# Performance work log

Hardware: AMD Instinct MI355X
Metric: run time of the kernel (lower is better)

Reference implementation:

```python
import jax, jax.numpy as jnp
import numpy as np


def setup_inputs() -> dict:
    key = jax.random.key(0)
    x = jax.random.uniform(key, (8, 3, 224, 224), dtype=jnp.float32)
    return {"x": x, "T": 100}


def reference(x, T):
    # normalize to [0, 1] using global min/max (as in the torch module)
    xn = (x - x.min()) / (x.max() - x.min() + 1e-8)
    # time-to-first-spike index per element, truncated like .long()
    spike_times = jnp.clip(((1.0 - xn) * (T - 1)).astype(jnp.int32), 0, T - 1)  # [B,C,H,W]
    # one-hot along the new time axis: spikes[b, t, ...] = 1 where t == spike_time
    t_axis = jnp.arange(T, dtype=jnp.int32)  # [T]
    spikes = (spike_times[:, None] == t_axis[None, :, None, None, None]).astype(jnp.float32)
    return spikes  # [B, T, C, H, W]
```

## Files before the change

kernel.cpp:

```cpp
#include <hip/hip_runtime.h>
#include <cfloat>

#define BLK 256
#define RED_BLOCKS 256
#define SPLIT 21

typedef float floatx4 __attribute__((ext_vector_type(4)));

__global__ void k_minmax_partial(const float* __restrict__ x, int n4,
                                 float* __restrict__ partial) {
    const float4* __restrict__ x4 = (const float4*)x;
    float mn = FLT_MAX, mx = -FLT_MAX;
    for (int i = blockIdx.x * blockDim.x + threadIdx.x; i < n4;
         i += gridDim.x * blockDim.x) {
        float4 v = x4[i];
        mn = fminf(mn, fminf(fminf(v.x, v.y), fminf(v.z, v.w)));
        mx = fmaxf(mx, fmaxf(fmaxf(v.x, v.y), fmaxf(v.z, v.w)));
    }
    for (int off = 32; off > 0; off >>= 1) {
        mn = fminf(mn, __shfl_down(mn, off, 64));
        mx = fmaxf(mx, __shfl_down(mx, off, 64));
    }
    __shared__ float smn[BLK / 64], smx[BLK / 64];
    int lane = threadIdx.x & 63;
    int w = threadIdx.x >> 6;
    if (lane == 0) { smn[w] = mn; smx[w] = mx; }
    __syncthreads();
    if (threadIdx.x == 0) {
        mn = smn[0]; mx = smx[0];
        for (int j = 1; j < BLK / 64; ++j) {
            mn = fminf(mn, smn[j]);
            mx = fmaxf(mx, smx[j]);
        }
        partial[2 * blockIdx.x]     = mn;
        partial[2 * blockIdx.x + 1] = mx;
    }
}

__global__ void k_spiketime(const float* __restrict__ x,
                            const float* __restrict__ partial,
                            const int* __restrict__ Tptr,
                            unsigned char* __restrict__ st, int n4) {
    __shared__ float smn[BLK / 64], smx[BLK / 64];
    __shared__ float sparams[2];
    {
        float mn = partial[2 * threadIdx.x];
        float mx = partial[2 * threadIdx.x + 1];
        for (int off = 32; off > 0; off >>= 1) {
            mn = fminf(mn, __shfl_down(mn, off, 64));
            mx = fmaxf(mx, __shfl_down(mx, off, 64));
        }
        int lane = threadIdx.x & 63;
        int w = threadIdx.x >> 6;
        if (lane == 0) { smn[w] = mn; smx[w] = mx; }
        __syncthreads();
        if (threadIdx.x == 0) {
            mn = smn[0]; mx = smx[0];
            for (int j = 1; j < BLK / 64; ++j) {
                mn = fminf(mn, smn[j]);
                mx = fmaxf(mx, smx[j]);
            }
            sparams[0] = mn;
            sparams[1] = (mx - mn) + 1e-8f;
        }
        __syncthreads();
    }
    int i = blockIdx.x * blockDim.x + threadIdx.x;
    if (i >= n4) return;
    const int T = Tptr[0];
    const float mn = sparams[0];
    const float d  = sparams[1];
    const float scaleT = (float)(T - 1);

    float4 v = ((const float4*)x)[i];
    int st0 = (int)((1.0f - (v.x - mn) / d) * scaleT);
    int st1 = (int)((1.0f - (v.y - mn) / d) * scaleT);
    int st2 = (int)((1.0f - (v.z - mn) / d) * scaleT);
    int st3 = (int)((1.0f - (v.w - mn) / d) * scaleT);
    st0 = min(max(st0, 0), T - 1);
    st1 = min(max(st1, 0), T - 1);
    st2 = min(max(st2, 0), T - 1);
    st3 = min(max(st3, 0), T - 1);

    uchar4 o;
    o.x = (unsigned char)st0;
    o.y = (unsigned char)st1;
    o.z = (unsigned char)st2;
    o.w = (unsigned char)st3;
    ((uchar4*)st)[i] = o;
}

__global__ void k_write(const unsigned char* __restrict__ st,
                        float* __restrict__ out,
                        int T, int CHW4, int PC) {
    int seg   = blockIdx.x;
    int part  = seg % SPLIT;
    int plane = seg / SPLIT;
    int t = plane % T;
    int b = plane / T;

    const uchar4* __restrict__ stp = (const uchar4*)st + (size_t)b * CHW4;
    floatx4* __restrict__ op = (floatx4*)out + (size_t)plane * CHW4;

    int j = part * PC + threadIdx.x;
    #pragma unroll
    for (int k = 0; k < 7; ++k, j += BLK) {
        uchar4 s = stp[j];
        floatx4 o;
        o.x = (s.x == t) ? 1.0f : 0.0f;
        o.y = (s.y == t) ? 1.0f : 0.0f;
        o.z = (s.z == t) ? 1.0f : 0.0f;
        o.w = (s.w == t) ? 1.0f : 0.0f;
        __builtin_nontemporal_store(o, op + j);
    }
}

extern "C" void kernel_launch(void* const* d_in, const int* in_sizes, int n_in,
                              void* d_out, int out_size, void* d_ws, size_t ws_size,
                              hipStream_t stream) {
    const float* x  = (const float*)d_in[0];
    const int* Tptr = (const int*)d_in[1];
    float* out      = (float*)d_out;

    const int n  = in_sizes[0];
    const int n4 = n / 4;
    const int B  = 8;
    const int T  = out_size / n;
    const int CHW  = n / B;
    const int CHW4 = CHW / 4;
    const int PC   = CHW4 / SPLIT;

    float* partial     = (float*)d_ws;
    unsigned char* st  = (unsigned char*)d_ws + 4096;

    k_minmax_partial<<<RED_BLOCKS, BLK, 0, stream>>>(x, n4, partial);

    int blocks = (n4 + BLK - 1) / BLK;
    k_spiketime<<<blocks, BLK, 0, stream>>>(x, partial, Tptr, st, n4);

    int wblocks = B * T * SPLIT;
    k_write<<<wblocks, BLK, 0, stream>>>(st, out, T, CHW4, PC);
}
```

Baseline: 478.4 us.

## Loop over time chunks per thread, reusing each spike-time load

The write kernel now assigns each thread one uchar4 of spike times and loops over a chunk of about ten time steps. It writes the one-hot float4 for each step, so the spike-time read is reused instead of reloaded per time plane. Non-temporal stores are replaced by ordinary stores. Each iteration writes a CHW-strided address, which changes the store access pattern and the grid size.

```diff
diff --git a/kernel.cpp b/kernel.cpp
--- a/kernel.cpp
+++ b/kernel.cpp
@@ -3,9 +3,7 @@
 
 #define BLK 256
 #define RED_BLOCKS 256
-#define SPLIT 21
-
-typedef float floatx4 __attribute__((ext_vector_type(4)));
+#define NCHUNK 10
 
 __global__ void k_minmax_partial(const float* __restrict__ x, int n4,
                                  float* __restrict__ partial) {
@@ -92,26 +90,31 @@
 
 __global__ void k_write(const unsigned char* __restrict__ st,
                         float* __restrict__ out,
-                        int T, int CHW4, int PC) {
-    int seg   = blockIdx.x;
-    int part  = seg % SPLIT;
-    int plane = seg / SPLIT;
-    int t = plane % T;
-    int b = plane / T;
+                        int T, int TC, int CHW4, int SEGS) {
+    int id = blockIdx.x;
+    int sg = id % SEGS;
+    int c  = (id / SEGS) % NCHUNK;
+    int b  = id / (SEGS * NCHUNK);
 
-    const uchar4* __restrict__ stp = (const uchar4*)st + (size_t)b * CHW4;
-    floatx4* __restrict__ op = (floatx4*)out + (size_t)plane * CHW4;
+    int j = sg * BLK + threadIdx.x;
+    if (j >= CHW4) return;
 
-    int j = part * PC + threadIdx.x;
-    #pragma unroll
-    for (int k = 0; k < 7; ++k, j += BLK) {
-        uchar4 s = stp[j];
-        floatx4 o;
-        o.x = (s.x == t) ? 1.0f : 0.0f;
-        o.y = (s.y == t) ? 1.0f : 0.0f;
-        o.z = (s.z == t) ? 1.0f : 0.0f;
-        o.w = (s.w == t) ? 1.0f : 0.0f;
-        __builtin_nontemporal_store(o, op + j);
+    uchar4 s = ((const uchar4*)st)[(size_t)b * CHW4 + j];
+    const int s0 = s.x, s1 = s.y, s2 = s.z, s3 = s.w;
+
+    const int t0 = c * TC;
+    const int t1 = min(t0 + TC, T);
+
+    float4* __restrict__ op =
+        (float4*)out + ((size_t)b * T + t0) * (size_t)CHW4 + j;
+
+    for (int t = t0; t < t1; ++t, op += CHW4) {
+        float4 o;
+        o.x = (s0 == t) ? 1.0f : 0.0f;
+        o.y = (s1 == t) ? 1.0f : 0.0f;
+        o.z = (s2 == t) ? 1.0f : 0.0f;
+        o.w = (s3 == t) ? 1.0f : 0.0f;
+        *op = o;
     }
 }
 
@@ -128,7 +131,6 @@
     const int T  = out_size / n;
     const int CHW  = n / B;
     const int CHW4 = CHW / 4;
-    const int PC   = CHW4 / SPLIT;
 
     float* partial     = (float*)d_ws;
     unsigned char* st  = (unsigned char*)d_ws + 4096;
@@ -138,6 +140,8 @@
     int blocks = (n4 + BLK - 1) / BLK;
     k_spiketime<<<blocks, BLK, 0, stream>>>(x, partial, Tptr, st, n4);
 
-    int wblocks = B * T * SPLIT;
-    k_write<<<wblocks, BLK, 0, stream>>>(st, out, T, CHW4, PC);
+    const int SEGS = (CHW4 + BLK - 1) / BLK;
+    const int TC   = (T + NCHUNK - 1) / NCHUNK;
+    int wblocks = B * NCHUNK * SEGS;
+    k_write<<<wblocks, BLK, 0, stream>>>(st, out, T, TC, CHW4, SEGS);
 }
```

Result: no change. 476.1 us (-0.5%).
